# Optimization experiments

Measured on AMD Instinct MI355X. Metric: run time of the kernel, lower is better.

The kernel has to match this reference:

```python
import jax, jax.numpy as jnp
import numpy as np

C = 4096
IN_DIM = 256
OUT_DIM = 64
H = 4
NEG_SLOPE = 0.2


def setup_inputs() -> dict:
    key = jax.random.key(0)
    k_x, k_adj, k_w, k_as, k_ad = jax.random.split(key, 5)
    x = jax.random.normal(k_x, (C, IN_DIM), dtype=jnp.float32)
    adj = jax.random.randint(k_adj, (C, C), 0, 2, dtype=jnp.int32)
    # xavier_uniform for Linear(in, out*H): bound = sqrt(6/(fan_in+fan_out))
    bw = float(np.sqrt(6.0 / (IN_DIM + OUT_DIM * H)))
    W = jax.random.uniform(k_w, (IN_DIM, OUT_DIM * H), minval=-bw, maxval=bw, dtype=jnp.float32)
    ba = float(np.sqrt(6.0 / (H + OUT_DIM)))
    a_src = jax.random.uniform(k_as, (H, OUT_DIM), minval=-ba, maxval=ba, dtype=jnp.float32)
    a_dst = jax.random.uniform(k_ad, (H, OUT_DIM), minval=-ba, maxval=ba, dtype=jnp.float32)
    return {"x": x, "adj": adj, "W": W, "a_src": a_src, "a_dst": a_dst}


def reference(x, adj, W, a_src, a_dst):
    # h: [C, H, D] -> h_heads: [H, C, D]
    h = (x @ W).reshape(C, H, OUT_DIM)
    h_heads = jnp.transpose(h, (1, 0, 2))
    # per-node additive attention logits: [H, C]
    alpha_src = jnp.einsum('hcd,hd->hc', h_heads, a_src)
    alpha_dst = jnp.einsum('hcd,hd->hc', h_heads, a_dst)
    # broadcast scores e: [H, C, C]
    e = alpha_src[:, :, None] + alpha_dst[:, None, :]
    e = jnp.where(e >= 0, e, NEG_SLOPE * e)  # LeakyReLU
    e = jnp.where(adj[None, :, :] == 0, -jnp.inf, e)
    attn = jax.nn.softmax(e, axis=-1)  # [H, C, C]
    out = jnp.einsum('hcj,hjd->hcd', attn, h_heads)  # [H, C, D]
    return jnp.transpose(out, (1, 0, 2)).reshape(C, H * OUT_DIM)
```

## Files before the change

### kernel.cpp

```cpp
#include <hip/hip_runtime.h>
#include <math.h>

#define CN 4096
#define KDIM 256
#define ND 256
#define NH 4
#define DD 64
#define NEG 0.2f
#define L2E 1.44269504f

typedef __attribute__((ext_vector_type(8))) short short8;
typedef __attribute__((ext_vector_type(4))) float floatx4;

union S8I4 { int i[4]; short8 s; };

__device__ inline unsigned bfbits_rne(float f) {
  unsigned u = __float_as_uint(f);
  u += 0x7fffu + ((u >> 16) & 1u);
  return u >> 16;
}
__device__ inline float bf2f(unsigned hi) { return __uint_as_float(hi << 16); }

__device__ inline int pack2_trunc(float a, float b) {
  return (int)__builtin_amdgcn_perm(__float_as_uint(b), __float_as_uint(a), 0x07060302u);
}

#define GLDS(gp, lp, sz)                                                        \
  __builtin_amdgcn_global_load_lds(                                             \
      (const __attribute__((address_space(1))) void*)(gp),                      \
      (__attribute__((address_space(3))) void*)(lp), (sz), 0, 0)

__global__ __launch_bounds__(256) void k_prep(const int* __restrict__ adj,
                                              unsigned long long* __restrict__ mbits,
                                              const float* __restrict__ W,
                                              unsigned short* __restrict__ WT_hi,
                                              unsigned short* __restrict__ WT_lo) {
  const int bx = blockIdx.x;
  const int t = threadIdx.x;
  if (bx < 4096) {
    const int w = t >> 6, lane = t & 63;
    const size_t base = ((size_t)(bx * 4 + w)) * 1024;
#pragma unroll 4
    for (int it = 0; it < 16; ++it) {
      const size_t idx = base + (size_t)it * 64 + lane;
      const unsigned long long m = __ballot(adj[idx] != 0);
      if (lane == 0) mbits[idx >> 6] = m;
    }
  } else {
    const int c = (bx - 4096) * 4 + (t >> 6);
    const int k0 = (t & 63) * 4;
    unsigned h[4], l[4];
#pragma unroll
    for (int j = 0; j < 4; ++j) {
      const float w = W[(size_t)(k0 + j) * ND + c];
      h[j] = bfbits_rne(w);
      l[j] = bfbits_rne(w - bf2f(h[j]));
    }
    uint2 vh, vl;
    vh.x = h[0] | (h[1] << 16); vh.y = h[2] | (h[3] << 16);
    vl.x = l[0] | (l[1] << 16); vl.y = l[2] | (l[3] << 16);
    *(uint2*)&WT_hi[(size_t)c * KDIM + k0] = vh;
    *(uint2*)&WT_lo[(size_t)c * KDIM + k0] = vl;
  }
}

__global__ __launch_bounds__(256, 2) void k_gemm_h(const float* __restrict__ x,
                                                   const unsigned short* __restrict__ WT_hi,
                                                   const unsigned short* __restrict__ WT_lo,
                                                   const float* __restrict__ a_src,
                                                   const float* __restrict__ a_dst,
                                                   unsigned short* __restrict__ hT,
                                                   float* __restrict__ asrc,
                                                   float* __restrict__ adst) {
  __shared__ __align__(16) unsigned short Whi_s[64 * 264];
  __shared__ __align__(16) unsigned short Wlo_s[64 * 264];
  const int t = threadIdx.x;
  const int lane = t & 63, ww = t >> 6;
  const int n = lane & 15, q = lane >> 4;
  const int head = blockIdx.x;
  const int i0 = blockIdx.y * 64 + ww * 16;
#pragma unroll
  for (int p = 0; p < 8; ++p) {
    const int s = p * 256 + t;
    const int c = s >> 5, kseg = s & 31;
    const size_t g = (size_t)(head * 64 + c) * KDIM + kseg * 8;
    *(short8*)&Whi_s[c * 264 + kseg * 8] = *(const short8*)(WT_hi + g);
    *(short8*)&Wlo_s[c * 264 + kseg * 8] = *(const short8*)(WT_lo + g);
  }
  const float* xr = x + (size_t)(i0 + n) * KDIM + q * 8;
  float4 xa = *(const float4*)(xr);
  float4 xb = *(const float4*)(xr + 4);
  __syncthreads();
  floatx4 acc[4] = {};
  for (int k0 = 0; k0 < KDIM; k0 += 32) {
    const float xs[8] = {xa.x, xa.y, xa.z, xa.w, xb.x, xb.y, xb.z, xb.w};
    if (k0 + 32 < KDIM) {
      xa = *(const float4*)(xr + k0 + 32);
      xb = *(const float4*)(xr + k0 + 36);
    }
    S8I4 Ah, Al;
#pragma unroll
    for (int e = 0; e < 4; ++e) {
      const unsigned h0 = bfbits_rne(xs[2 * e]), h1 = bfbits_rne(xs[2 * e + 1]);
      const float r0 = xs[2 * e] - bf2f(h0), r1 = xs[2 * e + 1] - bf2f(h1);
      Ah.i[e] = (int)(h0 | (h1 << 16));
      Al.i[e] = (int)(bfbits_rne(r0) | (bfbits_rne(r1) << 16));
    }
#pragma unroll
    for (int tt = 0; tt < 4; ++tt) {
      const int boff = (tt * 16 + n) * 264 + k0 + q * 8;
      const short8 Bh = *(const short8*)&Whi_s[boff];
      const short8 Bl = *(const short8*)&Wlo_s[boff];
      acc[tt] = __builtin_amdgcn_mfma_f32_16x16x32_bf16(Ah.s, Bh, acc[tt], 0, 0, 0);
      acc[tt] = __builtin_amdgcn_mfma_f32_16x16x32_bf16(Al.s, Bh, acc[tt], 0, 0, 0);
      acc[tt] = __builtin_amdgcn_mfma_f32_16x16x32_bf16(Ah.s, Bl, acc[tt], 0, 0, 0);
    }
  }
  unsigned short* hTb = hT + (size_t)head * DD * CN;
#pragma unroll
  for (int tt = 0; tt < 4; ++tt)
#pragma unroll
    for (int r = 0; r < 4; r += 2) {
      const unsigned d = bfbits_rne(acc[tt][r]) | (bfbits_rne(acc[tt][r + 1]) << 16);
      *(unsigned*)(hTb + (size_t)(tt * 16 + n) * CN + i0 + q * 4 + r) = d;
    }
  float ps[4] = {}, pd[4] = {};
#pragma unroll
  for (int tt = 0; tt < 4; ++tt) {
    const float as = a_src[head * DD + tt * 16 + n];
    const float ad = a_dst[head * DD + tt * 16 + n];
#pragma unroll
    for (int r = 0; r < 4; ++r) {
      ps[r] += acc[tt][r] * as;
      pd[r] += acc[tt][r] * ad;
    }
  }
#pragma unroll
  for (int off = 1; off < 16; off <<= 1)
#pragma unroll
    for (int r = 0; r < 4; ++r) {
      ps[r] += __shfl_xor(ps[r], off);
      pd[r] += __shfl_xor(pd[r], off);
    }
  if (n == 0) {
#pragma unroll
    for (int r = 0; r < 4; ++r) {
      asrc[head * CN + i0 + q * 4 + r] = ps[r] * L2E;
      adst[head * CN + i0 + q * 4 + r] = pd[r] * L2E;
    }
  }
}

__global__ __launch_bounds__(512, 4) void k_attn(const unsigned short* __restrict__ hT,
                                                 const unsigned* __restrict__ mbits32,
                                                 const float* __restrict__ asrc,
                                                 const float* __restrict__ adst,
                                                 float* __restrict__ out) {
  __shared__ __align__(16) char smem[8 * 2 * 4608];
  const int t = threadIdx.x;
  const int lane = t & 63, ww = t >> 6;
  const int n = lane & 15, q = lane >> 4;
  const int head = blockIdx.y;
  const int i0 = blockIdx.x * 32;
  const unsigned short* __restrict__ hTb = hT + (size_t)head * DD * CN;
  const float* __restrict__ adh = adst + head * CN;
  const int jbase = ww * 512;

  const float sp0 = asrc[head * CN + i0 + n];
  const float sp1 = asrc[head * CN + i0 + 16 + n];

  const unsigned hoff =
      (unsigned)(lane >> 2) * CN + (((lane & 3) ^ ((lane >> 3) & 3)) * 8);
  const unsigned mrow = (unsigned)(i0 + (lane & 31)) * 128;
  const unsigned arow = (unsigned)(lane & 31);
  char* const wbase = smem + ww * 2 * 4608;

  short8 ONES;
#pragma unroll
  for (int u = 0; u < 8; ++u) ONES[u] = (short)0x3F80;

  floatx4 acc[2][4] = {};
  floatx4 accz[2] = {};

  auto ISSUE = [&](int b, int j0) {
    char* base = wbase + b * 4608;
#pragma unroll
    for (int g = 0; g < 4; ++g)
      GLDS(hTb + (size_t)(g * 16) * CN + hoff + j0, base + g * 1024, 16);
    GLDS(mbits32 + mrow + (j0 >> 5), base + 4096, 4);
    GLDS(adh + j0 + arow, base + 4352, 4);
  };

  ISSUE(0, jbase);
  for (int c = 0; c < 16; ++c) {
    if (c < 15) {
      ISSUE((c + 1) & 1, jbase + (c + 1) * 32);
      asm volatile("s_waitcnt vmcnt(6)" ::: "memory");
    } else {
      asm volatile("s_waitcnt vmcnt(0)" ::: "memory");
    }
    const char* base = wbase + (c & 1) * 4608;
    short8 B[4];
#pragma unroll
    for (int tt = 0; tt < 4; ++tt)
      B[tt] = *(const short8*)(base + (tt * 16 + n) * 64 +
                               ((q ^ ((n >> 1) & 3)) << 4));
    const unsigned m0 = *(const unsigned*)(base + 4096 + n * 4);
    const unsigned m1 = *(const unsigned*)(base + 4096 + (16 + n) * 4);
    const float* adl = (const float*)(base + 4352);
    const float4 a0 = *(const float4*)(adl + q * 8);
    const float4 a1 = *(const float4*)(adl + q * 8 + 4);
    const float ade[8] = {a0.x, a0.y, a0.z, a0.w, a1.x, a1.y, a1.z, a1.w};
#pragma unroll
    for (int rg = 0; rg < 2; ++rg) {
      const unsigned mbyte = ((rg ? m1 : m0) >> (q * 8)) & 255u;
      const float sp = rg ? sp1 : sp0;
      float fv[8];
#pragma unroll
      for (int e = 0; e < 8; ++e) {
        float xv = sp + ade[e];
        xv = fmaxf(xv, NEG * xv);
        xv = ((mbyte >> e) & 1u) ? xv : -1e38f;
        fv[e] = __builtin_amdgcn_exp2f(xv);
      }
      S8I4 A;
#pragma unroll
      for (int e = 0; e < 4; ++e) A.i[e] = pack2_trunc(fv[2 * e], fv[2 * e + 1]);
      accz[rg] = __builtin_amdgcn_mfma_f32_16x16x32_bf16(A.s, ONES, accz[rg], 0, 0, 0);
#pragma unroll
      for (int tt = 0; tt < 4; ++tt)
        acc[rg][tt] =
            __builtin_amdgcn_mfma_f32_16x16x32_bf16(A.s, B[tt], acc[rg][tt], 0, 0, 0);
    }
  }

  __syncthreads();
  float* red = (float*)smem;
  if (ww > 0) {
    float* rb = red + (ww - 1) * 2560;
#pragma unroll
    for (int rg = 0; rg < 2; ++rg) {
#pragma unroll
      for (int tt = 0; tt < 4; ++tt)
#pragma unroll
        for (int r = 0; r < 4; ++r)
          rb[(rg * 20 + tt * 4 + r) * 64 + lane] = acc[rg][tt][r];
#pragma unroll
      for (int r = 0; r < 4; ++r) rb[(rg * 20 + 16 + r) * 64 + lane] = accz[rg][r];
    }
  }
  __syncthreads();
  if (ww == 0) {
#pragma unroll
    for (int s = 0; s < 7; ++s) {
      const float* rb = red + s * 2560;
#pragma unroll
      for (int rg = 0; rg < 2; ++rg) {
#pragma unroll
        for (int tt = 0; tt < 4; ++tt)
#pragma unroll
          for (int r = 0; r < 4; ++r)
            acc[rg][tt][r] += rb[(rg * 20 + tt * 4 + r) * 64 + lane];
#pragma unroll
        for (int r = 0; r < 4; ++r) accz[rg][r] += rb[(rg * 20 + 16 + r) * 64 + lane];
      }
    }
#pragma unroll
    for (int rg = 0; rg < 2; ++rg)
#pragma unroll
      for (int r = 0; r < 4; ++r) {
        const float iz = 1.0f / accz[rg][r];
        float* orow = out + (size_t)(i0 + rg * 16 + q * 4 + r) * ND + head * DD + n;
#pragma unroll
        for (int tt = 0; tt < 4; ++tt) orow[tt * 16] = acc[rg][tt][r] * iz;
      }
  }
}

extern "C" void kernel_launch(void* const* d_in, const int* in_sizes, int n_in,
                              void* d_out, int out_size, void* d_ws, size_t ws_size,
                              hipStream_t stream) {
  const float* x = (const float*)d_in[0];
  const int* adj = (const int*)d_in[1];
  const float* W = (const float*)d_in[2];
  const float* a_src = (const float*)d_in[3];
  const float* a_dst = (const float*)d_in[4];
  float* out = (float*)d_out;

  unsigned short* hT = (unsigned short*)d_ws;
  float* asrc = (float*)(hT + (size_t)NH * DD * CN);
  float* adst = asrc + (size_t)NH * CN;
  unsigned short* WT_hi = (unsigned short*)(adst + (size_t)NH * CN);
  unsigned short* WT_lo = WT_hi + (size_t)ND * KDIM;
  unsigned long long* mbits = (unsigned long long*)(WT_lo + (size_t)ND * KDIM);

  k_prep<<<dim3(4096 + ND / 4), 256, 0, stream>>>(adj, mbits, W, WT_hi, WT_lo);
  k_gemm_h<<<dim3(NH, CN / 64), 256, 0, stream>>>(x, WT_hi, WT_lo, a_src, a_dst,
                                                  hT, asrc, adst);
  k_attn<<<dim3(CN / 32, NH), 512, 0, stream>>>(hT, (const unsigned*)mbits,
                                                asrc, adst, out);
}
```

Measured before the change: 154.7 us.

## Factor exp of LeakyReLU scores into per-node exponentials and fuse GEMM with mask prep

Because exp2 is monotonic, exp2(leaky(s+d)) equals max(exp2(s)exp2(d), exp2(0.2s)exp2(0.2d)). The change precomputes per-node exponential pairs for rows and columns, so the attention inner loop uses multiplies and a max instead of exp2 per element. The h GEMM now runs inside the same launch as the adjacency bitmask pass, reading W straight from global memory instead of staging it in LDS, and W conversion gets its own small kernel. The softmax is unnormalised with no max subtraction, and both this and the product form can overflow or underflow for large logits.

```diff
diff --git a/kernel.cpp b/kernel.cpp
--- a/kernel.cpp
+++ b/kernel.cpp
@@ -30,74 +30,61 @@
       (const __attribute__((address_space(1))) void*)(gp),                      \
       (__attribute__((address_space(3))) void*)(lp), (sz), 0, 0)
 
-__global__ __launch_bounds__(256) void k_prep(const int* __restrict__ adj,
-                                              unsigned long long* __restrict__ mbits,
-                                              const float* __restrict__ W,
+__global__ __launch_bounds__(256) void k_wcvt(const float* __restrict__ W,
                                               unsigned short* __restrict__ WT_hi,
                                               unsigned short* __restrict__ WT_lo) {
+  const int t = threadIdx.x;
+  const int c = blockIdx.x * 4 + (t >> 6);
+  const int k0 = (t & 63) * 4;
+  unsigned h[4], l[4];
+#pragma unroll
+  for (int j = 0; j < 4; ++j) {
+    const float w = W[(size_t)(k0 + j) * ND + c];
+    h[j] = bfbits_rne(w);
+    l[j] = bfbits_rne(w - bf2f(h[j]));
+  }
+  uint2 vh, vl;
+  vh.x = h[0] | (h[1] << 16); vh.y = h[2] | (h[3] << 16);
+  vl.x = l[0] | (l[1] << 16); vl.y = l[2] | (l[3] << 16);
+  *(uint2*)&WT_hi[(size_t)c * KDIM + k0] = vh;
+  *(uint2*)&WT_lo[(size_t)c * KDIM + k0] = vl;
+}
+
+__global__ __launch_bounds__(256) void k_pre(const int* __restrict__ adj,
+                                             unsigned long long* __restrict__ mbits,
+                                             const float* __restrict__ x,
+                                             const unsigned short* __restrict__ WT_hi,
+                                             const unsigned short* __restrict__ WT_lo,
+                                             const float* __restrict__ a_src,
+                                             const float* __restrict__ a_dst,
+                                             unsigned short* __restrict__ hT,
+                                             float2* __restrict__ Erow,
+                                             float2* __restrict__ Ecol) {
   const int bx = blockIdx.x;
   const int t = threadIdx.x;
-  if (bx < 4096) {
+  if (bx >= 256) {
     const int w = t >> 6, lane = t & 63;
-    const size_t base = ((size_t)(bx * 4 + w)) * 1024;
+    const size_t base = ((size_t)(bx - 256)) * 4096 + (size_t)w * 1024;
 #pragma unroll 4
     for (int it = 0; it < 16; ++it) {
       const size_t idx = base + (size_t)it * 64 + lane;
       const unsigned long long m = __ballot(adj[idx] != 0);
       if (lane == 0) mbits[idx >> 6] = m;
     }
-  } else {
-    const int c = (bx - 4096) * 4 + (t >> 6);
-    const int k0 = (t & 63) * 4;
-    unsigned h[4], l[4];
-#pragma unroll
-    for (int j = 0; j < 4; ++j) {
-      const float w = W[(size_t)(k0 + j) * ND + c];
-      h[j] = bfbits_rne(w);
-      l[j] = bfbits_rne(w - bf2f(h[j]));
-    }
-    uint2 vh, vl;
-    vh.x = h[0] | (h[1] << 16); vh.y = h[2] | (h[3] << 16);
-    vl.x = l[0] | (l[1] << 16); vl.y = l[2] | (l[3] << 16);
-    *(uint2*)&WT_hi[(size_t)c * KDIM + k0] = vh;
-    *(uint2*)&WT_lo[(size_t)c * KDIM + k0] = vl;
-  }
-}
-
-__global__ __launch_bounds__(256, 2) void k_gemm_h(const float* __restrict__ x,
-                                                   const unsigned short* __restrict__ WT_hi,
-                                                   const unsigned short* __restrict__ WT_lo,
-                                                   const float* __restrict__ a_src,
-                                                   const float* __restrict__ a_dst,
-                                                   unsigned short* __restrict__ hT,
-                                                   float* __restrict__ asrc,
-                                                   float* __restrict__ adst) {
-  __shared__ __align__(16) unsigned short Whi_s[64 * 264];
-  __shared__ __align__(16) unsigned short Wlo_s[64 * 264];
-  const int t = threadIdx.x;
+    return;
+  }
   const int lane = t & 63, ww = t >> 6;
   const int n = lane & 15, q = lane >> 4;
-  const int head = blockIdx.x;
-  const int i0 = blockIdx.y * 64 + ww * 16;
-#pragma unroll
-  for (int p = 0; p < 8; ++p) {
-    const int s = p * 256 + t;
-    const int c = s >> 5, kseg = s & 31;
-    const size_t g = (size_t)(head * 64 + c) * KDIM + kseg * 8;
-    *(short8*)&Whi_s[c * 264 + kseg * 8] = *(const short8*)(WT_hi + g);
-    *(short8*)&Wlo_s[c * 264 + kseg * 8] = *(const short8*)(WT_lo + g);
-  }
+  const int head = bx >> 6;
+  const int c0 = head * DD;
+  const int i0 = (bx & 63) * 64 + ww * 16;
   const float* xr = x + (size_t)(i0 + n) * KDIM + q * 8;
-  float4 xa = *(const float4*)(xr);
-  float4 xb = *(const float4*)(xr + 4);
-  __syncthreads();
   floatx4 acc[4] = {};
+#pragma unroll 2
   for (int k0 = 0; k0 < KDIM; k0 += 32) {
+    const float4 xa = *(const float4*)(xr + k0);
+    const float4 xb = *(const float4*)(xr + k0 + 4);
     const float xs[8] = {xa.x, xa.y, xa.z, xa.w, xb.x, xb.y, xb.z, xb.w};
-    if (k0 + 32 < KDIM) {
-      xa = *(const float4*)(xr + k0 + 32);
-      xb = *(const float4*)(xr + k0 + 36);
-    }
     S8I4 Ah, Al;
 #pragma unroll
     for (int e = 0; e < 4; ++e) {
@@ -108,9 +95,9 @@
     }
 #pragma unroll
     for (int tt = 0; tt < 4; ++tt) {
-      const int boff = (tt * 16 + n) * 264 + k0 + q * 8;
-      const short8 Bh = *(const short8*)&Whi_s[boff];
-      const short8 Bl = *(const short8*)&Wlo_s[boff];
+      const size_t boff = (size_t)(c0 + tt * 16 + n) * KDIM + k0 + q * 8;
+      const short8 Bh = *(const short8*)(WT_hi + boff);
+      const short8 Bl = *(const short8*)(WT_lo + boff);
       acc[tt] = __builtin_amdgcn_mfma_f32_16x16x32_bf16(Ah.s, Bh, acc[tt], 0, 0, 0);
       acc[tt] = __builtin_amdgcn_mfma_f32_16x16x32_bf16(Al.s, Bh, acc[tt], 0, 0, 0);
       acc[tt] = __builtin_amdgcn_mfma_f32_16x16x32_bf16(Ah.s, Bl, acc[tt], 0, 0, 0);
@@ -145,16 +132,20 @@
   if (n == 0) {
 #pragma unroll
     for (int r = 0; r < 4; ++r) {
-      asrc[head * CN + i0 + q * 4 + r] = ps[r] * L2E;
-      adst[head * CN + i0 + q * 4 + r] = pd[r] * L2E;
+      const int i = i0 + q * 4 + r;
+      const float as_ = ps[r] * L2E, ad_ = pd[r] * L2E;
+      Erow[head * CN + i] = make_float2(__builtin_amdgcn_exp2f(as_),
+                                        __builtin_amdgcn_exp2f(NEG * as_));
+      Ecol[head * CN + i] = make_float2(__builtin_amdgcn_exp2f(ad_),
+                                        __builtin_amdgcn_exp2f(NEG * ad_));
     }
   }
 }
 
 __global__ __launch_bounds__(512, 4) void k_attn(const unsigned short* __restrict__ hT,
                                                  const unsigned* __restrict__ mbits32,
-                                                 const float* __restrict__ asrc,
-                                                 const float* __restrict__ adst,
+                                                 const float2* __restrict__ Erow,
+                                                 const float2* __restrict__ Ecol,
                                                  float* __restrict__ out) {
   __shared__ __align__(16) char smem[8 * 2 * 4608];
   const int t = threadIdx.x;
@@ -163,16 +154,15 @@
   const int head = blockIdx.y;
   const int i0 = blockIdx.x * 32;
   const unsigned short* __restrict__ hTb = hT + (size_t)head * DD * CN;
-  const float* __restrict__ adh = adst + head * CN;
+  const float* __restrict__ ecf = (const float*)(Ecol + (size_t)head * CN);
   const int jbase = ww * 512;
 
-  const float sp0 = asrc[head * CN + i0 + n];
-  const float sp1 = asrc[head * CN + i0 + 16 + n];
+  const float2 es0 = Erow[head * CN + i0 + n];
+  const float2 es1 = Erow[head * CN + i0 + 16 + n];
 
   const unsigned hoff =
       (unsigned)(lane >> 2) * CN + (((lane & 3) ^ ((lane >> 3) & 3)) * 8);
   const unsigned mrow = (unsigned)(i0 + (lane & 31)) * 128;
-  const unsigned arow = (unsigned)(lane & 31);
   char* const wbase = smem + ww * 2 * 4608;
 
   short8 ONES;
@@ -188,7 +178,7 @@
     for (int g = 0; g < 4; ++g)
       GLDS(hTb + (size_t)(g * 16) * CN + hoff + j0, base + g * 1024, 16);
     GLDS(mbits32 + mrow + (j0 >> 5), base + 4096, 4);
-    GLDS(adh + j0 + arow, base + 4352, 4);
+    GLDS(ecf + j0 * 2 + lane, base + 4352, 4);
   };
 
   ISSUE(0, jbase);
@@ -207,30 +197,31 @@
                                ((q ^ ((n >> 1) & 3)) << 4));
     const unsigned m0 = *(const unsigned*)(base + 4096 + n * 4);
     const unsigned m1 = *(const unsigned*)(base + 4096 + (16 + n) * 4);
-    const float* adl = (const float*)(base + 4352);
-    const float4 a0 = *(const float4*)(adl + q * 8);
-    const float4 a1 = *(const float4*)(adl + q * 8 + 4);
-    const float ade[8] = {a0.x, a0.y, a0.z, a0.w, a1.x, a1.y, a1.z, a1.w};
+    const unsigned mb0 = (m0 >> (q * 8)) & 255u;
+    const unsigned mb1 = (m1 >> (q * 8)) & 255u;
+    const float4* adl4 = (const float4*)(base + 4352);
+    S8I4 A[2];
+#pragma unroll
+    for (int g = 0; g < 4; ++g) {
+      const float4 v = adl4[q * 4 + g];
+#pragma unroll
+      for (int rg = 0; rg < 2; ++rg) {
+        const float2 es = rg ? es1 : es0;
+        const unsigned mb = rg ? mb1 : mb0;
+        float w0 = fmaxf(es.x * v.x, es.y * v.y);
+        float w1 = fmaxf(es.x * v.z, es.y * v.w);
+        w0 = ((mb >> (2 * g)) & 1u) ? w0 : 0.0f;
+        w1 = ((mb >> (2 * g + 1)) & 1u) ? w1 : 0.0f;
+        A[rg].i[g] = pack2_trunc(w0, w1);
+      }
+    }
 #pragma unroll
     for (int rg = 0; rg < 2; ++rg) {
-      const unsigned mbyte = ((rg ? m1 : m0) >> (q * 8)) & 255u;
-      const float sp = rg ? sp1 : sp0;
-      float fv[8];
-#pragma unroll
-      for (int e = 0; e < 8; ++e) {
-        float xv = sp + ade[e];
-        xv = fmaxf(xv, NEG * xv);
-        xv = ((mbyte >> e) & 1u) ? xv : -1e38f;
-        fv[e] = __builtin_amdgcn_exp2f(xv);
-      }
-      S8I4 A;
-#pragma unroll
-      for (int e = 0; e < 4; ++e) A.i[e] = pack2_trunc(fv[2 * e], fv[2 * e + 1]);
-      accz[rg] = __builtin_amdgcn_mfma_f32_16x16x32_bf16(A.s, ONES, accz[rg], 0, 0, 0);
+      accz[rg] = __builtin_amdgcn_mfma_f32_16x16x32_bf16(A[rg].s, ONES, accz[rg], 0, 0, 0);
 #pragma unroll
       for (int tt = 0; tt < 4; ++tt)
         acc[rg][tt] =
-            __builtin_amdgcn_mfma_f32_16x16x32_bf16(A.s, B[tt], acc[rg][tt], 0, 0, 0);
+            __builtin_amdgcn_mfma_f32_16x16x32_bf16(A[rg].s, B[tt], acc[rg][tt], 0, 0, 0);
     }
   }
 
@@ -288,15 +279,15 @@
   float* out = (float*)d_out;
 
   unsigned short* hT = (unsigned short*)d_ws;
-  float* asrc = (float*)(hT + (size_t)NH * DD * CN);
-  float* adst = asrc + (size_t)NH * CN;
-  unsigned short* WT_hi = (unsigned short*)(adst + (size_t)NH * CN);
+  float2* Erow = (float2*)(hT + (size_t)NH * DD * CN);
+  float2* Ecol = Erow + (size_t)NH * CN;
+  unsigned short* WT_hi = (unsigned short*)(Ecol + (size_t)NH * CN);
   unsigned short* WT_lo = WT_hi + (size_t)ND * KDIM;
   unsigned long long* mbits = (unsigned long long*)(WT_lo + (size_t)ND * KDIM);
 
-  k_prep<<<dim3(4096 + ND / 4), 256, 0, stream>>>(adj, mbits, W, WT_hi, WT_lo);
-  k_gemm_h<<<dim3(NH, CN / 64), 256, 0, stream>>>(x, WT_hi, WT_lo, a_src, a_dst,
-                                                  hT, asrc, adst);
+  k_wcvt<<<dim3(ND / 4), 256, 0, stream>>>(W, WT_hi, WT_lo);
+  k_pre<<<dim3(256 + CN), 256, 0, stream>>>(adj, mbits, x, WT_hi, WT_lo,
+                                            a_src, a_dst, hT, Erow, Ecol);
   k_attn<<<dim3(CN / 32, NH), 512, 0, stream>>>(hT, (const unsigned*)mbits,
-                                                asrc, adst, out);
-}
+                                                Erow, Ecol, out);
+}
```

Measured after the change: 158.5 us. 1.02x slower.
